# Kernel optimization log

Hardware: AMD Instinct MI355X
Metric: run time of the kernel (lower is better)

The kernel has to match this reference:

```python
import jax, jax.numpy as jnp
import numpy as np

E, H, V, P, RAW = 512, 1024, 12000, 36, 2048
B, L = 128, 21

def setup_inputs() -> dict:
    key = jax.random.key(0)
    ks = jax.random.split(key, 16)
    n = lambda k, sh: (0.02 * jax.random.normal(k, sh)).astype(jnp.float32)
    z = lambda sh: jnp.zeros(sh, jnp.float32)
    return {
        "images_features": jax.random.normal(ks[0], (B, P, RAW), dtype=jnp.float32),
        "encoded_captions": jax.random.randint(ks[1], (B, L), 0, V),
        "caption_lengths": L,
        "W_img": n(ks[2], (RAW, H)), "b_img": z((H,)),
        "W_glob": n(ks[3], (H, E)), "b_glob": z((E,)),
        "W_ih1": n(ks[4], (2 * E + H, 4 * H)), "W_hh1": n(ks[5], (H, 4 * H)),
        "b_ih1": z((4 * H,)), "b_hh1": z((4 * H,)),
        "Wx_gate": n(ks[6], (2 * E + H, H)), "bx_gate": z((H,)),
        "Wh_gate": n(ks[7], (H, H)), "bh_gate": z((H,)),
        "W_ih2": n(ks[8], (2 * H, 4 * H)), "W_hh2": n(ks[9], (H, 4 * H)),
        "b_ih2": z((4 * H,)), "b_hh2": z((4 * H,)),
        "Wv": n(ks[10], (H, P)), "bv": z((P,)),
        "Ws": n(ks[11], (H, P)), "bs": z((P,)),
        "Wg": n(ks[12], (H, P)),
        "wh": n(ks[13], (P,)),
        "emb": n(ks[14], (V, E)),
        "W_fc": n(ks[15], (H, V)), "b_fc": z((V,)),
    }

def _lstm(x, h, c, W_ih, W_hh, b_ih, b_hh):
    # torch LSTMCell gate order: i, f, g, o
    g = x @ W_ih + b_ih + h @ W_hh + b_hh
    i, f, gg, o = jnp.split(g, 4, axis=-1)
    c_new = jax.nn.sigmoid(f) * c + jax.nn.sigmoid(i) * jnp.tanh(gg)
    h_new = jax.nn.sigmoid(o) * jnp.tanh(c_new)
    return h_new, c_new

def reference(images_features, encoded_captions, caption_lengths, W_img, b_img,
              W_glob, b_glob, W_ih1, W_hh1, b_ih1, b_hh1, Wx_gate, bx_gate,
              Wh_gate, bh_gate, W_ih2, W_hh2, b_ih2, b_hh2, Wv, bv, Ws, bs,
              Wg, wh, emb, W_fc, b_fc):
    Bsz = images_features.shape[0]
    Hd = W_hh1.shape[0]
    T = int(caption_lengths) - 1
    Vfeat = jax.nn.relu(images_features @ W_img + b_img)            # (B,P,H)
    glob = jax.nn.relu(jnp.mean(Vfeat, axis=1) @ W_glob + b_glob)   # (B,E)
    img_proj = Vfeat @ Wv + bv                                      # (B,P,P) loop-invariant
    word_embs = emb[encoded_captions[:, :T]]                        # (B,T,E)

    def step(carry, we):
        h1, c1, h2, c2 = carry
        xt = jnp.concatenate([h2, glob, we], axis=-1)               # (B, H+2E)
        h1n, c1n = _lstm(xt, h1, c1, W_ih1, W_hh1, b_ih1, b_hh1)
        sen_gate = jax.nn.sigmoid(xt @ Wx_gate + bx_gate + h1 @ Wh_gate + bh_gate)
        st = sen_gate * jnp.tanh(c1n)                               # visual sentinel
        ht_proj = h1n @ Wg                                          # (B,P)
        z = jnp.tanh(img_proj + ht_proj[:, :, None]) @ wh           # (B,P)
        alpha = jax.nn.softmax(z, axis=1)                           # (B,P)
        context = jnp.einsum('bp,bph->bh', alpha, Vfeat)            # (B,H)
        att_vs = jnp.tanh(st @ Ws + bs + ht_proj) @ wh              # (B,)
        alpha_hat = jax.nn.softmax(jnp.concatenate([z, att_vs[:, None]], axis=1), axis=1)
        beta = alpha_hat[:, -1:]                                    # (B,1)
        c_hat = beta * st + (1.0 - beta) * context
        h2n, c2n = _lstm(jnp.concatenate([c_hat, h1n], axis=-1), h2, c2,
                         W_ih2, W_hh2, b_ih2, b_hh2)
        score = (c_hat + h2n) @ W_fc + b_fc                         # (B,V)
        return (h1n, c1n, h2n, c2n), (score, alpha, beta)

    zeros = jnp.zeros((Bsz, Hd), images_features.dtype)
    init = (zeros, zeros, zeros, zeros)
    _, (preds, alphas, betas) = jax.lax.scan(step, init, jnp.swapaxes(word_embs, 0, 1))
    return (jnp.swapaxes(preds, 0, 1),   # (B,T,V)
            jnp.swapaxes(alphas, 0, 1),  # (B,T,P)
            jnp.swapaxes(betas, 0, 1))   # (B,T,1)
```

## Files before the change

### kernel.cpp

```cpp
#include <hip/hip_runtime.h>
#include <hip/hip_bf16.h>
#include <math.h>

typedef __attribute__((ext_vector_type(4))) float f32x4;
typedef __attribute__((ext_vector_type(8))) short bf16x8;

constexpr int kB = 128, kT = 20, kH = 1024, kE = 512, kP = 36, kRaw = 2048, kV = 12000;

__device__ __forceinline__ float sigf(float x) { return 1.0f / (1.0f + expf(-x)); }

#define AS1C const __attribute__((address_space(1))) void*
#define AS3P __attribute__((address_space(3))) void*

constexpr int NZ1 = 2 * kB * kH / 4;
constexpr int NZ2 = 2 * kB * kH * 2 / 16;
constexpr int NCV = kB * kP * kRaw / 4;
constexpr int NPV = 64 * 1024 * 2 / 16;
constexpr int NPF = 32 * 1024 * 2 / 16;
constexpr int NPB = 5120;
constexpr int NGE = kB * kT * kE;

__global__ __launch_bounds__(256) void prep_small(
    float* c1z, uint4* h1z, const float* images, __hip_bfloat16* imagesb,
    uint4* wtv, uint4* wtfc_pad,
    const float* b_ih1, const float* b_hh1, const float* bx, const float* bh,
    const float* b_ih2, const float* b_hh2, float* bias_g1, float* bias_g2,
    const int* caps, const float* emb, __hip_bfloat16* wembb) {
  long idx = (long)blockIdx.x * 256 + threadIdx.x;
  if (idx < NZ1) { reinterpret_cast<float4*>(c1z)[idx] = make_float4(0, 0, 0, 0); return; }
  idx -= NZ1;
  if (idx < NZ2) { h1z[idx] = make_uint4(0, 0, 0, 0); return; }
  idx -= NZ2;
  if (idx < NCV) {
    float4 v = reinterpret_cast<const float4*>(images)[idx];
    __hip_bfloat16* d = imagesb + idx * 4;
    d[0] = __float2bfloat16(v.x); d[1] = __float2bfloat16(v.y);
    d[2] = __float2bfloat16(v.z); d[3] = __float2bfloat16(v.w);
    return;
  }
  idx -= NCV;
  if (idx < NPV) { wtv[idx] = make_uint4(0, 0, 0, 0); return; }
  idx -= NPV;
  if (idx < NPF) { wtfc_pad[idx] = make_uint4(0, 0, 0, 0); return; }
  idx -= NPF;
  if (idx < NPB) {
    int i = (int)idx;
    if (i < 4096) {
      bias_g1[i] = b_ih1[i] + b_hh1[i];
      bias_g2[i] = b_ih2[i] + b_hh2[i];
    } else {
      bias_g1[i] = bx[i - 4096] + bh[i - 4096];
    }
    return;
  }
  idx -= NPB;
  if (idx < NGE) {
    int e = (int)(idx % kE);
    int bt = (int)(idx / kE);
    int t = bt % kT;
    int b = bt / kT;
    int tok = caps[b * (kT + 1) + t];
    wembb[idx] = __float2bfloat16(emb[(size_t)tok * kE + e]);
  }
}

struct TJob {
  const float* src; __hip_bfloat16* dst;
  int ld_src, K, N, lddst, koff, noff, blk_off, nbx;
};
struct TAll { TJob job[11]; int njobs; int total_blocks; };

__global__ __launch_bounds__(256) void transpose_all(TAll ta) {
  __shared__ float t[32][33];
  int bid = blockIdx.x;
  int ji = 0;
  while (ji + 1 < ta.njobs && bid >= ta.job[ji + 1].blk_off) ++ji;
  const TJob& J = ta.job[ji];
  int lbid = bid - J.blk_off;
  int n0 = (lbid % J.nbx) * 32, k0 = (lbid / J.nbx) * 32;
  int tx = threadIdx.x & 31, ty = threadIdx.x >> 5;
  #pragma unroll
  for (int i = 0; i < 32; i += 8) {
    int k = k0 + ty + i, n = n0 + tx;
    t[ty + i][tx] = (k < J.K && n < J.N) ? J.src[(size_t)k * J.ld_src + n] : 0.0f;
  }
  __syncthreads();
  #pragma unroll
  for (int i = 0; i < 32; i += 8) {
    int n = n0 + ty + i, k = k0 + tx;
    if (n < J.N && k < J.K)
      J.dst[(size_t)(n + J.noff) * J.lddst + k + J.koff] = __float2bfloat16(t[tx][ty + i]);
  }
}

struct SegB { const __hip_bfloat16* A; int lda; int kstart; int kend; };
struct GemmBArgs {
  SegB seg[4]; int nseg;
  const __hip_bfloat16* WT; int ldk;
  const float* bias;
  float* C; __hip_bfloat16* C16; int ldc; int N; int Ktot; int act;
};

__global__ __launch_bounds__(256) void gemm_bf16(GemmBArgs ga) {
  __shared__ char lds[98304];
  const int bm = blockIdx.y * 64;
  const int bn = blockIdx.x * 64;
  const int tid = threadIdx.x;
  const int lane = tid & 63;
  const int w = tid >> 6;
  const int wr = w >> 1, wc = w & 1;

  int rowS[4], scbS[4], dstS[4];
  #pragma unroll
  for (int j = 0; j < 4; ++j) {
    int off = ((j * 4 + w) * 64 + lane) * 16;
    int row = off >> 8, colb = off & 255;
    rowS[j] = row;
    scbS[j] = colb ^ ((row & 7) << 4);
    dstS[j] = (j * 4 + w) * 1024;
  }

  f32x4 acc[2][2] = {};
  const int nit = ga.Ktot >> 7;

  auto stage = [&](int it, int buf) {
    const int k0 = it << 7;
    int si = 0;
    while (k0 >= ga.seg[si].kend) ++si;
    const __hip_bfloat16* Aseg = ga.seg[si].A;
    const int lda = ga.seg[si].lda;
    const int ks = k0 - ga.seg[si].kstart;
    char* baseA = lds + buf * 32768;
    char* baseB = baseA + 16384;
    #pragma unroll
    for (int j = 0; j < 4; ++j) {
      const __hip_bfloat16* sA = Aseg + (size_t)(bm + rowS[j]) * lda + ks + (scbS[j] >> 1);
      __builtin_amdgcn_global_load_lds((AS1C)sA, (AS3P)(baseA + dstS[j]), 16, 0, 0);
      const __hip_bfloat16* sB = ga.WT + (size_t)(bn + rowS[j]) * ga.ldk + k0 + (scbS[j] >> 1);
      __builtin_amdgcn_global_load_lds((AS1C)sB, (AS3P)(baseB + dstS[j]), 16, 0, 0);
    }
  };

  auto compute = [&](int buf) {
    const char* baseA = lds + buf * 32768;
    const char* baseB = baseA + 16384;
    #pragma unroll
    for (int kk = 0; kk < 4; ++kk) {
      bf16x8 a[2], b[2];
      #pragma unroll
      for (int f = 0; f < 2; ++f) {
        int row = wr * 32 + f * 16 + (lane & 15);
        int cb = kk * 64 + (lane >> 4) * 16;
        a[f] = *(const bf16x8*)(baseA + row * 256 + (cb ^ ((row & 7) << 4)));
        int nl = wc * 32 + f * 16 + (lane & 15);
        b[f] = *(const bf16x8*)(baseB + nl * 256 + (cb ^ ((nl & 7) << 4)));
      }
      #pragma unroll
      for (int fm = 0; fm < 2; ++fm)
        #pragma unroll
        for (int fn = 0; fn < 2; ++fn)
          acc[fm][fn] = __builtin_amdgcn_mfma_f32_16x16x32_bf16(a[fm], b[fn], acc[fm][fn], 0, 0, 0);
    }
  };

  stage(0, 0);
  stage(1, 1);
  asm volatile("s_waitcnt vmcnt(8)" ::: "memory");
  __builtin_amdgcn_s_barrier();
  int cbuf = 0;
  for (int it = 0; it < nit; ++it) {
    if (it + 2 < nit) {
      int sb = cbuf + 2; if (sb >= 3) sb -= 3;
      stage(it + 2, sb);
    }
    compute(cbuf);
    if (it + 1 < nit) {
      if (it + 2 < nit) asm volatile("s_waitcnt vmcnt(8)" ::: "memory");
      else              asm volatile("s_waitcnt vmcnt(0)" ::: "memory");
      __builtin_amdgcn_s_barrier();
    }
    ++cbuf; if (cbuf == 3) cbuf = 0;
  }

  #pragma unroll
  for (int fm = 0; fm < 2; ++fm) {
    int rbase = bm + wr * 32 + fm * 16 + (lane >> 4) * 4;
    #pragma unroll
    for (int fn = 0; fn < 2; ++fn) {
      int col = bn + wc * 32 + fn * 16 + (lane & 15);
      if (col >= ga.N) continue;
      float bv = ga.bias ? ga.bias[col] : 0.0f;
      #pragma unroll
      for (int j = 0; j < 4; ++j) {
        float v = acc[fm][fn][j] + bv;
        if (ga.act == 1) v = fmaxf(v, 0.0f);
        size_t off = (size_t)(rbase + j) * ga.ldc + col;
        if (ga.C) ga.C[off] = v;
        if (ga.C16) ga.C16[off] = __float2bfloat16(v);
      }
    }
  }
}

struct G128Args {
  const __hip_bfloat16* A; int lda;
  const __hip_bfloat16* WT; int ldk;
  const float* bias;
  float* C; __hip_bfloat16* C16; int ldc; int N; int Ktot; int act; int cmap;
};

__global__ __launch_bounds__(256) void gemm128(G128Args ga) {
  __shared__ char lds[98304];
  const int gx = gridDim.x;
  const int nwg = gx * gridDim.y;
  int bid = blockIdx.y * gx + blockIdx.x;
  int q = nwg >> 3, r = nwg & 7;
  int xc = bid & 7, yq = bid >> 3;
  int swz = (xc < r ? xc * (q + 1) : r * (q + 1) + (xc - r) * q) + yq;
  const int bn = (swz % gx) * 128;
  const int bm = (swz / gx) * 128;

  const int tid = threadIdx.x;
  const int lane = tid & 63;
  const int w = tid >> 6;
  const int wr = w >> 1, wc = w & 1;

  int rowS[4], scbS[4], dstS[4];
  #pragma unroll
  for (int j = 0; j < 4; ++j) {
    int off = ((j * 4 + w) * 64 + lane) * 16;
    int row = off >> 7, colb = off & 127;
    rowS[j] = row;
    scbS[j] = colb ^ ((row & 7) << 4);
    dstS[j] = (j * 4 + w) * 1024;
  }

  f32x4 acc[4][4] = {};
  const int nit = ga.Ktot >> 6;

  auto stage = [&](int it, int buf) {
    const int k0 = it << 6;
    char* baseA = lds + buf * 32768;
    char* baseB = baseA + 16384;
    #pragma unroll
    for (int j = 0; j < 4; ++j) {
      const __hip_bfloat16* sA = ga.A + (size_t)(bm + rowS[j]) * ga.lda + k0 + (scbS[j] >> 1);
      __builtin_amdgcn_global_load_lds((AS1C)sA, (AS3P)(baseA + dstS[j]), 16, 0, 0);
      const __hip_bfloat16* sB = ga.WT + (size_t)(bn + rowS[j]) * ga.ldk + k0 + (scbS[j] >> 1);
      __builtin_amdgcn_global_load_lds((AS1C)sB, (AS3P)(baseB + dstS[j]), 16, 0, 0);
    }
  };

  auto compute = [&](int buf) {
    const char* baseA = lds + buf * 32768;
    const char* baseB = baseA + 16384;
    #pragma unroll
    for (int kk = 0; kk < 2; ++kk) {
      bf16x8 a[4], b[4];
      int cb = kk * 64 + (lane >> 4) * 16;
      #pragma unroll
      for (int f = 0; f < 4; ++f) {
        int row = wr * 64 + f * 16 + (lane & 15);
        a[f] = *(const bf16x8*)(baseA + row * 128 + (cb ^ ((row & 7) << 4)));
        int nl = wc * 64 + f * 16 + (lane & 15);
        b[f] = *(const bf16x8*)(baseB + nl * 128 + (cb ^ ((nl & 7) << 4)));
      }
      #pragma unroll
      for (int fm = 0; fm < 4; ++fm)
        #pragma unroll
        for (int fn = 0; fn < 4; ++fn)
          acc[fm][fn] = __builtin_amdgcn_mfma_f32_16x16x32_bf16(a[fm], b[fn], acc[fm][fn], 0, 0, 0);
    }
  };

  stage(0, 0);
  stage(1, 1);
  asm volatile("s_waitcnt vmcnt(8)" ::: "memory");
  __builtin_amdgcn_s_barrier();
  int cbuf = 0;
  for (int it = 0; it < nit; ++it) {
    if (it + 2 < nit) {
      int sb = cbuf + 2; if (sb >= 3) sb -= 3;
      stage(it + 2, sb);
    }
    compute(cbuf);
    if (it + 1 < nit) {
      if (it + 2 < nit) asm volatile("s_waitcnt vmcnt(8)" ::: "memory");
      else              asm volatile("s_waitcnt vmcnt(0)" ::: "memory");
      __builtin_amdgcn_s_barrier();
    }
    ++cbuf; if (cbuf == 3) cbuf = 0;
  }

  #pragma unroll
  for (int fm = 0; fm < 4; ++fm) {
    int rbase = bm + wr * 64 + fm * 16 + (lane >> 4) * 4;
    #pragma unroll
    for (int fn = 0; fn < 4; ++fn) {
      int col = bn + wc * 64 + fn * 16 + (lane & 15);
      if (col >= ga.N) continue;
      float bv = ga.bias ? ga.bias[col] : 0.0f;
      #pragma unroll
      for (int j = 0; j < 4; ++j) {
        float v = acc[fm][fn][j] + bv;
        if (ga.act == 1) v = fmaxf(v, 0.0f);
        int m = rbase + j;
        size_t off = ga.cmap == 1
            ? (size_t)(m & 127) * ga.ldc + (size_t)(m >> 7) * kV + col
            : (size_t)m * ga.ldc + col;
        if (ga.C) ga.C[off] = v;
        if (ga.C16) ga.C16[off] = __float2bfloat16(v);
      }
    }
  }
}

__global__ __launch_bounds__(256) void mean_p(const float* __restrict__ Vfeat,
                                              __hip_bfloat16* __restrict__ meanVb) {
  int idx = blockIdx.x * 256 + threadIdx.x;
  if (idx >= kB * kH) return;
  int b = idx >> 10, h = idx & 1023;
  float sm = 0.0f;
  for (int p = 0; p < kP; ++p) sm += Vfeat[((size_t)b * kP + p) * kH + h];
  meanVb[idx] = __float2bfloat16(sm * (1.0f / kP));
}

__global__ __launch_bounds__(256) void step1_fused(
    const float* __restrict__ g, float* __restrict__ c1,
    __hip_bfloat16* __restrict__ h1b,
    const float* __restrict__ img_proj, const float* __restrict__ Vfeat,
    const float* __restrict__ Wg, const float* __restrict__ Ws,
    const float* __restrict__ bs, const float* __restrict__ wh,
    float* __restrict__ c_hat, __hip_bfloat16* __restrict__ c_hatb,
    float* __restrict__ out_alphas, float* __restrict__ out_betas, int t) {
  const int b = blockIdx.x;
  const int tid = threadIdx.x;
  const int lane = tid & 63;
  const int w = tid >> 6;
  __shared__ float sh_h1[kH];
  __shared__ float sh_st[kH];
  __shared__ float wsum[4][36];
  __shared__ float htp[36];
  __shared__ float stp[36];
  __shared__ float alpha[kP];
  __shared__ float sred[4];

  const float* gr = g + (size_t)b * 5120;
  #pragma unroll
  for (int i = 0; i < 4; ++i) {
    int h = tid + i * 256;
    float ig = sigf(gr[h]);
    float fg = sigf(gr[kH + h]);
    float gg = tanhf(gr[2 * kH + h]);
    float og = sigf(gr[3 * kH + h]);
    int idx = b * kH + h;
    float c = fg * c1[idx] + ig * gg;
    float tc = tanhf(c);
    float hn = og * tc;
    c1[idx] = c;
    h1b[idx] = __float2bfloat16(hn);
    sh_h1[h] = hn;
    sh_st[h] = sigf(gr[4 * kH + h]) * tc;
  }
  __syncthreads();

  #pragma unroll
  for (int pass = 0; pass < 2; ++pass) {
    const float* vec = pass == 0 ? sh_h1 : sh_st;
    const float* W = pass == 0 ? Wg : Ws;
    float pg[36];
    #pragma unroll
    for (int j = 0; j < 36; ++j) pg[j] = 0.0f;
    #pragma unroll
    for (int i = 0; i < 4; ++i) {
      int hh = tid + i * 256;
      float hv = vec[hh];
      const float4* wrow = reinterpret_cast<const float4*>(W + (size_t)hh * 36);
      #pragma unroll
      for (int r = 0; r < 9; ++r) {
        float4 wv = wrow[r];
        pg[4 * r + 0] = fmaf(hv, wv.x, pg[4 * r + 0]);
        pg[4 * r + 1] = fmaf(hv, wv.y, pg[4 * r + 1]);
        pg[4 * r + 2] = fmaf(hv, wv.z, pg[4 * r + 2]);
        pg[4 * r + 3] = fmaf(hv, wv.w, pg[4 * r + 3]);
      }
    }
    #pragma unroll
    for (int j = 0; j < 36; ++j) {
      float v = pg[j];
      #pragma unroll
      for (int off = 32; off > 0; off >>= 1) v += __shfl_down(v, off, 64);
      if (lane == 0) wsum[w][j] = v;
    }
    __syncthreads();
    if (tid < 36) {
      float s = wsum[0][tid] + wsum[1][tid] + wsum[2][tid] + wsum[3][tid];
      if (pass == 0) htp[tid] = s; else stp[tid] = s;
    }
    __syncthreads();
  }

  if (w == 0) {
    float zz_r = -3.0e38f;
    if (lane < kP) {
      const float* ip = img_proj + ((size_t)b * kP + lane) * kP;
      float acc = 0.0f;
      #pragma unroll
      for (int j = 0; j < kP; ++j) acc = fmaf(tanhf(ip[j] + htp[j]), wh[j], acc);
      zz_r = acc;
    }
    float m = zz_r;
    #pragma unroll
    for (int off = 32; off > 0; off >>= 1) m = fmaxf(m, __shfl_xor(m, off, 64));
    float e = (lane < kP) ? expf(zz_r - m) : 0.0f;
    float s = e;
    #pragma unroll
    for (int off = 32; off > 0; off >>= 1) s += __shfl_xor(s, off, 64);
    if (lane < kP) alpha[lane] = e / s;
    if (lane == 0) { sred[2] = m; sred[3] = s; }
  } else if (w == 1) {
    float tv = 0.0f;
    if (lane < kP) tv = tanhf(stp[lane] + bs[lane] + htp[lane]) * wh[lane];
    #pragma unroll
    for (int off = 32; off > 0; off >>= 1) tv += __shfl_xor(tv, off, 64);
    if (lane == 0) sred[0] = tv;
  }
  __syncthreads();
  if (tid == 0) {
    float av = sred[0], m = sred[2], s = sred[3];
    float m2 = fmaxf(m, av);
    float eb = expf(av - m2);
    float beta = eb / (s * expf(m - m2) + eb);
    sred[1] = beta;
    out_betas[b * kT + t] = beta;
  }
  __syncthreads();
  if (tid < kP) out_alphas[((size_t)b * kT + t) * kP + tid] = alpha[tid];
  const float beta = sred[1];
  #pragma unroll
  for (int i = 0; i < 4; ++i) {
    int h = tid + i * 256;
    float ctx = 0.0f;
    for (int p = 0; p < kP; ++p) ctx = fmaf(alpha[p], Vfeat[((size_t)b * kP + p) * kH + h], ctx);
    float v = beta * sh_st[h] + (1.0f - beta) * ctx;
    c_hat[(size_t)b * kH + h] = v;
    c_hatb[(size_t)b * kH + h] = __float2bfloat16(v);
  }
}

__global__ __launch_bounds__(256) void lstm2_elem(const float* __restrict__ g,
                                                  float* __restrict__ c2,
                                                  __hip_bfloat16* __restrict__ h2b,
                                                  const float* __restrict__ c_hat,
                                                  __hip_bfloat16* __restrict__ sbufb) {
  int idx = blockIdx.x * 256 + threadIdx.x;
  if (idx >= kB * kH) return;
  int b = idx >> 10, h = idx & 1023;
  const float* gr = g + (size_t)b * 4 * kH;
  float ig = sigf(gr[h]);
  float fg = sigf(gr[kH + h]);
  float gg = tanhf(gr[2 * kH + h]);
  float og = sigf(gr[3 * kH + h]);
  float c = fg * c2[idx] + ig * gg;
  float hn = og * tanhf(c);
  c2[idx] = c;
  h2b[idx] = __float2bfloat16(hn);
  sbufb[idx] = __float2bfloat16(c_hat[idx] + hn);
}

extern "C" void kernel_launch(void* const* d_in, const int* in_sizes, int n_in,
                              void* d_out, int out_size, void* d_ws, size_t ws_size,
                              hipStream_t stream) {
  const float* images  = (const float*)d_in[0];
  const int*   caps    = (const int*)d_in[1];
  const float* W_img   = (const float*)d_in[3];
  const float* b_img   = (const float*)d_in[4];
  const float* W_glob  = (const float*)d_in[5];
  const float* b_glob  = (const float*)d_in[6];
  const float* W_ih1   = (const float*)d_in[7];
  const float* W_hh1   = (const float*)d_in[8];
  const float* b_ih1   = (const float*)d_in[9];
  const float* b_hh1   = (const float*)d_in[10];
  const float* Wx_gate = (const float*)d_in[11];
  const float* bx_gate = (const float*)d_in[12];
  const float* Wh_gate = (const float*)d_in[13];
  const float* bh_gate = (const float*)d_in[14];
  const float* W_ih2   = (const float*)d_in[15];
  const float* W_hh2   = (const float*)d_in[16];
  const float* b_ih2   = (const float*)d_in[17];
  const float* b_hh2   = (const float*)d_in[18];
  const float* Wv      = (const float*)d_in[19];
  const float* bv      = (const float*)d_in[20];
  const float* Ws_     = (const float*)d_in[21];
  const float* bs_     = (const float*)d_in[22];
  const float* Wg      = (const float*)d_in[23];
  const float* wh      = (const float*)d_in[24];
  const float* emb     = (const float*)d_in[25];
  const float* W_fc    = (const float*)d_in[26];
  const float* b_fc    = (const float*)d_in[27];

  float* out = (float*)d_out;
  float* out_alphas = out + (size_t)kB * kT * kV;
  float* out_betas  = out_alphas + (size_t)kB * kT * kP;

  char* base = (char*)d_ws;
  auto alloc = [&](size_t bytes) {
    char* p = base;
    base += (bytes + 255) & ~(size_t)255;
    return p;
  };
  float*          Vfeat   = (float*)alloc((size_t)kB * kP * kH * 4);
  __hip_bfloat16* Vfeatb  = (__hip_bfloat16*)alloc((size_t)kB * kP * kH * 2);
  __hip_bfloat16* imagesb = (__hip_bfloat16*)alloc((size_t)kB * kP * kRaw * 2);
  __hip_bfloat16* WTg1    = (__hip_bfloat16*)alloc((size_t)5120 * 3072 * 2);
  __hip_bfloat16* WTg2    = (__hip_bfloat16*)alloc((size_t)4096 * 3072 * 2);
  __hip_bfloat16* WTfc    = (__hip_bfloat16*)alloc((size_t)12032 * 1024 * 2);
  __hip_bfloat16* WTimg   = (__hip_bfloat16*)alloc((size_t)1024 * 2048 * 2);
  __hip_bfloat16* WTglob  = (__hip_bfloat16*)alloc((size_t)512 * 1024 * 2);
  __hip_bfloat16* WTv     = (__hip_bfloat16*)alloc((size_t)64 * 1024 * 2);
  __hip_bfloat16* wembb   = (__hip_bfloat16*)alloc((size_t)kB * kT * kE * 2);
  float*          img_proj= (float*)alloc((size_t)kB * kP * kP * 4);
  __hip_bfloat16* globb   = (__hip_bfloat16*)alloc((size_t)kB * kE * 2);
  __hip_bfloat16* meanVb  = (__hip_bfloat16*)alloc((size_t)kB * kH * 2);
  float*          c1      = (float*)alloc((size_t)2 * kB * kH * 4);
  float*          c2      = c1 + kB * kH;
  __hip_bfloat16* h1b     = (__hip_bfloat16*)alloc((size_t)2 * kB * kH * 2);
  __hip_bfloat16* h2b     = h1b + kB * kH;
  float*          g1out   = (float*)alloc((size_t)kB * 5120 * 4);
  float*          chat    = (float*)alloc((size_t)kB * kH * 4);
  __hip_bfloat16* chatb   = (__hip_bfloat16*)alloc((size_t)kB * kH * 2);
  __hip_bfloat16* sbufall = (__hip_bfloat16*)alloc((size_t)kT * kB * kH * 2);
  float*          bias_g1 = (float*)alloc(5120 * 4);
  float*          bias_g2 = (float*)alloc(4096 * 4);

  {
    long total = (long)NZ1 + NZ2 + NCV + NPV + NPF + NPB + NGE;
    int blocks = (int)((total + 255) / 256);
    prep_small<<<blocks, 256, 0, stream>>>(
        c1, (uint4*)h1b, images, imagesb, (uint4*)WTv,
        (uint4*)(WTfc + (size_t)12000 * 1024),
        b_ih1, b_hh1, bx_gate, bh_gate, b_ih2, b_hh2, bias_g1, bias_g2,
        caps, emb, wembb);
  }
  {
    TAll ta = {};
    int off = 0, j = 0;
    auto add = [&](const float* src, int ldsrc, int K, int N, __hip_bfloat16* dst,
                   int lddst, int koff, int noff) {
      int nbx = (N + 31) / 32, nby = (K + 31) / 32;
      ta.job[j] = {src, dst, ldsrc, K, N, lddst, koff, noff, off, nbx};
      off += nbx * nby;
      ++j;
    };
    add(W_img,   kH,     kRaw, kH,     WTimg,  kRaw, 0, 0);
    add(W_glob,  kE,     kH,   kE,     WTglob, kH,   0, 0);
    add(Wv,      kP,     kH,   kP,     WTv,    kH,   0, 0);
    add(W_ih1,   4 * kH, 2048, 4 * kH, WTg1,   3072, 0, 0);
    add(W_hh1,   4 * kH, 1024, 4 * kH, WTg1,   3072, 2048, 0);
    add(Wx_gate, kH,     2048, kH,     WTg1,   3072, 0, 4096);
    add(Wh_gate, kH,     1024, kH,     WTg1,   3072, 2048, 4096);
    add(W_ih2,   4 * kH, 2048, 4 * kH, WTg2,   3072, 0, 0);
    add(W_hh2,   4 * kH, 1024, 4 * kH, WTg2,   3072, 2048, 0);
    add(W_fc,    kV,     kH,   kV,     WTfc,   kH,   0, 0);
    ta.njobs = j;
    ta.total_blocks = off;
    transpose_all<<<off, 256, 0, stream>>>(ta);
  }

  {
    G128Args ga = {};
    ga.A = imagesb; ga.lda = kRaw; ga.WT = WTimg; ga.ldk = kRaw; ga.bias = b_img;
    ga.C = Vfeat; ga.C16 = Vfeatb; ga.ldc = kH; ga.N = kH; ga.Ktot = kRaw;
    ga.act = 1; ga.cmap = 0;
    gemm128<<<dim3(kH / 128, kB * kP / 128), 256, 0, stream>>>(ga);
  }
  mean_p<<<(kB * kH + 255) / 256, 256, 0, stream>>>(Vfeat, meanVb);
  {
    GemmBArgs ga = {};
    ga.seg[0] = {meanVb, kH, 0, kH};
    ga.nseg = 1; ga.WT = WTglob; ga.ldk = kH; ga.bias = b_glob;
    ga.C = nullptr; ga.C16 = globb; ga.ldc = kE; ga.N = kE; ga.Ktot = kH; ga.act = 1;
    gemm_bf16<<<dim3(kE / 64, kB / 64), 256, 0, stream>>>(ga);
  }
  {
    GemmBArgs ga = {};
    ga.seg[0] = {Vfeatb, kH, 0, kH};
    ga.nseg = 1; ga.WT = WTv; ga.ldk = kH; ga.bias = bv;
    ga.C = img_proj; ga.C16 = nullptr; ga.ldc = kP; ga.N = kP; ga.Ktot = kH; ga.act = 0;
    gemm_bf16<<<dim3(1, kB * kP / 64), 256, 0, stream>>>(ga);
  }

  for (int t = 0; t < kT; ++t) {
    {
      GemmBArgs ga = {};
      ga.seg[0] = {h2b, kH, 0, kH};
      ga.seg[1] = {globb, kE, kH, kH + kE};
      ga.seg[2] = {wembb + (size_t)t * kE, kT * kE, kH + kE, 2048};
      ga.seg[3] = {h1b, kH, 2048, 3072};
      ga.nseg = 4; ga.WT = WTg1; ga.ldk = 3072; ga.bias = bias_g1;
      ga.C = g1out; ga.C16 = nullptr; ga.ldc = 5120; ga.N = 5120; ga.Ktot = 3072; ga.act = 0;
      gemm_bf16<<<dim3(5120 / 64, kB / 64), 256, 0, stream>>>(ga);
    }
    step1_fused<<<kB, 256, 0, stream>>>(g1out, c1, h1b, img_proj, Vfeat,
                                        Wg, Ws_, bs_, wh, chat, chatb,
                                        out_alphas, out_betas, t);
    {
      GemmBArgs ga = {};
      ga.seg[0] = {chatb, kH, 0, kH};
      ga.seg[1] = {h1b, kH, kH, 2048};
      ga.seg[2] = {h2b, kH, 2048, 3072};
      ga.nseg = 3; ga.WT = WTg2; ga.ldk = 3072; ga.bias = bias_g2;
      ga.C = g1out; ga.C16 = nullptr; ga.ldc = 4096; ga.N = 4096; ga.Ktot = 3072; ga.act = 0;
      gemm_bf16<<<dim3(4096 / 64, kB / 64), 256, 0, stream>>>(ga);
    }
    lstm2_elem<<<(kB * kH + 255) / 256, 256, 0, stream>>>(
        g1out, c2, h2b, chat, sbufall + (size_t)t * kB * kH);
  }

  {
    G128Args ga = {};
    ga.A = sbufall; ga.lda = kH; ga.WT = WTfc; ga.ldk = kH; ga.bias = b_fc;
    ga.C = out; ga.C16 = nullptr; ga.ldc = kT * kV; ga.N = kV; ga.Ktot = kH;
    ga.act = 0; ga.cmap = 1;
    gemm128<<<dim3(12032 / 128, kT * kB / 128), 256, 0, stream>>>(ga);
  }
}
```

Baseline: 1.829 ms.

## Split-K the per-step gate GEMMs and move to double-buffered LDS

The two recurrent gate GEMMs now launch with a grid z of 2. Each half covers half the K range and writes its partial sums to a separate output slab, and the bias add moves into the following elementwise kernels, which sum the two slabs. This is meant to double the workgroup count for these small 128-row GEMMs, which otherwise fill few CUs. Both GEMM kernels also drop from triple to double buffering (64 KB of LDS) with an extra barrier per iteration, which may allow higher occupancy but shortens prefetch depth and adds extra global traffic for the partial slabs.

```diff
diff --git a/kernel.cpp b/kernel.cpp
--- a/kernel.cpp
+++ b/kernel.cpp
@@ -98,11 +98,11 @@
   SegB seg[4]; int nseg;
   const __hip_bfloat16* WT; int ldk;
   const float* bias;
-  float* C; __hip_bfloat16* C16; int ldc; int N; int Ktot; int act;
+  float* C; __hip_bfloat16* C16; int ldc; int N; int Ktot; int act; int zstride;
 };
 
 __global__ __launch_bounds__(256) void gemm_bf16(GemmBArgs ga) {
-  __shared__ char lds[98304];
+  __shared__ char lds[65536];
   const int bm = blockIdx.y * 64;
   const int bn = blockIdx.x * 64;
   const int tid = threadIdx.x;
@@ -121,7 +121,10 @@
   }
 
   f32x4 acc[2][2] = {};
-  const int nit = ga.Ktot >> 7;
+  const int nz = gridDim.z;
+  const int nit = (ga.Ktot >> 7) / nz;
+  const int it0 = blockIdx.z * nit;
+  float* C = ga.C + (size_t)blockIdx.z * ga.zstride;
 
   auto stage = [&](int it, int buf) {
     const int k0 = it << 7;
@@ -163,23 +166,21 @@
     }
   };
 
-  stage(0, 0);
-  stage(1, 1);
+  stage(it0, 0);
+  stage(it0 + 1, 1);
   asm volatile("s_waitcnt vmcnt(8)" ::: "memory");
   __builtin_amdgcn_s_barrier();
-  int cbuf = 0;
-  for (int it = 0; it < nit; ++it) {
-    if (it + 2 < nit) {
-      int sb = cbuf + 2; if (sb >= 3) sb -= 3;
-      stage(it + 2, sb);
-    }
-    compute(cbuf);
-    if (it + 1 < nit) {
-      if (it + 2 < nit) asm volatile("s_waitcnt vmcnt(8)" ::: "memory");
-      else              asm volatile("s_waitcnt vmcnt(0)" ::: "memory");
+  int cur = 0;
+  for (int i = 0; i < nit; ++i) {
+    compute(cur);
+    __builtin_amdgcn_s_barrier();
+    if (i + 2 < nit) stage(it0 + i + 2, cur);
+    if (i + 1 < nit) {
+      if (i + 2 < nit) asm volatile("s_waitcnt vmcnt(8)" ::: "memory");
+      else             asm volatile("s_waitcnt vmcnt(0)" ::: "memory");
       __builtin_amdgcn_s_barrier();
     }
-    ++cbuf; if (cbuf == 3) cbuf = 0;
+    cur ^= 1;
   }
 
   #pragma unroll
@@ -195,7 +196,7 @@
         float v = acc[fm][fn][j] + bv;
         if (ga.act == 1) v = fmaxf(v, 0.0f);
         size_t off = (size_t)(rbase + j) * ga.ldc + col;
-        if (ga.C) ga.C[off] = v;
+        if (ga.C) C[off] = v;
         if (ga.C16) ga.C16[off] = __float2bfloat16(v);
       }
     }
@@ -210,7 +211,7 @@
 };
 
 __global__ __launch_bounds__(256) void gemm128(G128Args ga) {
-  __shared__ char lds[98304];
+  __shared__ char lds[65536];
   const int gx = gridDim.x;
   const int nwg = gx * gridDim.y;
   int bid = blockIdx.y * gx + blockIdx.x;
@@ -277,19 +278,17 @@
   stage(1, 1);
   asm volatile("s_waitcnt vmcnt(8)" ::: "memory");
   __builtin_amdgcn_s_barrier();
-  int cbuf = 0;
-  for (int it = 0; it < nit; ++it) {
-    if (it + 2 < nit) {
-      int sb = cbuf + 2; if (sb >= 3) sb -= 3;
-      stage(it + 2, sb);
-    }
-    compute(cbuf);
-    if (it + 1 < nit) {
-      if (it + 2 < nit) asm volatile("s_waitcnt vmcnt(8)" ::: "memory");
-      else              asm volatile("s_waitcnt vmcnt(0)" ::: "memory");
+  int cur = 0;
+  for (int i = 0; i < nit; ++i) {
+    compute(cur);
+    __builtin_amdgcn_s_barrier();
+    if (i + 2 < nit) stage(i + 2, cur);
+    if (i + 1 < nit) {
+      if (i + 2 < nit) asm volatile("s_waitcnt vmcnt(8)" ::: "memory");
+      else             asm volatile("s_waitcnt vmcnt(0)" ::: "memory");
       __builtin_amdgcn_s_barrier();
     }
-    ++cbuf; if (cbuf == 3) cbuf = 0;
+    cur ^= 1;
   }
 
   #pragma unroll
@@ -325,9 +324,10 @@
   meanVb[idx] = __float2bfloat16(sm * (1.0f / kP));
 }
 
+constexpr int kSlab1 = kB * 5120;
 __global__ __launch_bounds__(256) void step1_fused(
-    const float* __restrict__ g, float* __restrict__ c1,
-    __hip_bfloat16* __restrict__ h1b,
+    const float* __restrict__ g, const float* __restrict__ bias_g1,
+    float* __restrict__ c1, __hip_bfloat16* __restrict__ h1b,
     const float* __restrict__ img_proj, const float* __restrict__ Vfeat,
     const float* __restrict__ Wg, const float* __restrict__ Ws,
     const float* __restrict__ bs, const float* __restrict__ wh,
@@ -345,14 +345,15 @@
   __shared__ float alpha[kP];
   __shared__ float sred[4];
 
-  const float* gr = g + (size_t)b * 5120;
+  const float* gr0 = g + (size_t)b * 5120;
+  const float* gr1 = gr0 + kSlab1;
   #pragma unroll
   for (int i = 0; i < 4; ++i) {
     int h = tid + i * 256;
-    float ig = sigf(gr[h]);
-    float fg = sigf(gr[kH + h]);
-    float gg = tanhf(gr[2 * kH + h]);
-    float og = sigf(gr[3 * kH + h]);
+    float ig = sigf(gr0[h]           + gr1[h]           + bias_g1[h]);
+    float fg = sigf(gr0[kH + h]      + gr1[kH + h]      + bias_g1[kH + h]);
+    float gg = tanhf(gr0[2 * kH + h] + gr1[2 * kH + h]  + bias_g1[2 * kH + h]);
+    float og = sigf(gr0[3 * kH + h]  + gr1[3 * kH + h]  + bias_g1[3 * kH + h]);
     int idx = b * kH + h;
     float c = fg * c1[idx] + ig * gg;
     float tc = tanhf(c);
@@ -360,7 +361,7 @@
     c1[idx] = c;
     h1b[idx] = __float2bfloat16(hn);
     sh_h1[h] = hn;
-    sh_st[h] = sigf(gr[4 * kH + h]) * tc;
+    sh_st[h] = sigf(gr0[4 * kH + h] + gr1[4 * kH + h] + bias_g1[4 * kH + h]) * tc;
   }
   __syncthreads();
 
@@ -448,7 +449,9 @@
   }
 }
 
+constexpr int kSlab2 = kB * 4096;
 __global__ __launch_bounds__(256) void lstm2_elem(const float* __restrict__ g,
+                                                  const float* __restrict__ bias_g2,
                                                   float* __restrict__ c2,
                                                   __hip_bfloat16* __restrict__ h2b,
                                                   const float* __restrict__ c_hat,
@@ -456,11 +459,12 @@
   int idx = blockIdx.x * 256 + threadIdx.x;
   if (idx >= kB * kH) return;
   int b = idx >> 10, h = idx & 1023;
-  const float* gr = g + (size_t)b * 4 * kH;
-  float ig = sigf(gr[h]);
-  float fg = sigf(gr[kH + h]);
-  float gg = tanhf(gr[2 * kH + h]);
-  float og = sigf(gr[3 * kH + h]);
+  const float* gr0 = g + (size_t)b * 4 * kH;
+  const float* gr1 = gr0 + kSlab2;
+  float ig = sigf(gr0[h]           + gr1[h]           + bias_g2[h]);
+  float fg = sigf(gr0[kH + h]      + gr1[kH + h]      + bias_g2[kH + h]);
+  float gg = tanhf(gr0[2 * kH + h] + gr1[2 * kH + h]  + bias_g2[2 * kH + h]);
+  float og = sigf(gr0[3 * kH + h]  + gr1[3 * kH + h]  + bias_g2[3 * kH + h]);
   float c = fg * c2[idx] + ig * gg;
   float hn = og * tanhf(c);
   c2[idx] = c;
@@ -526,7 +530,7 @@
   float*          c2      = c1 + kB * kH;
   __hip_bfloat16* h1b     = (__hip_bfloat16*)alloc((size_t)2 * kB * kH * 2);
   __hip_bfloat16* h2b     = h1b + kB * kH;
-  float*          g1out   = (float*)alloc((size_t)kB * 5120 * 4);
+  float*          g1out   = (float*)alloc((size_t)2 * kB * 5120 * 4);
   float*          chat    = (float*)alloc((size_t)kB * kH * 4);
   __hip_bfloat16* chatb   = (__hip_bfloat16*)alloc((size_t)kB * kH * 2);
   __hip_bfloat16* sbufall = (__hip_bfloat16*)alloc((size_t)kT * kB * kH * 2);
@@ -580,14 +584,14 @@
     ga.seg[0] = {meanVb, kH, 0, kH};
     ga.nseg = 1; ga.WT = WTglob; ga.ldk = kH; ga.bias = b_glob;
     ga.C = nullptr; ga.C16 = globb; ga.ldc = kE; ga.N = kE; ga.Ktot = kH; ga.act = 1;
-    gemm_bf16<<<dim3(kE / 64, kB / 64), 256, 0, stream>>>(ga);
+    gemm_bf16<<<dim3(kE / 64, kB / 64, 1), 256, 0, stream>>>(ga);
   }
   {
     GemmBArgs ga = {};
     ga.seg[0] = {Vfeatb, kH, 0, kH};
     ga.nseg = 1; ga.WT = WTv; ga.ldk = kH; ga.bias = bv;
     ga.C = img_proj; ga.C16 = nullptr; ga.ldc = kP; ga.N = kP; ga.Ktot = kH; ga.act = 0;
-    gemm_bf16<<<dim3(1, kB * kP / 64), 256, 0, stream>>>(ga);
+    gemm_bf16<<<dim3(1, kB * kP / 64, 1), 256, 0, stream>>>(ga);
   }
 
   for (int t = 0; t < kT; ++t) {
@@ -597,11 +601,12 @@
       ga.seg[1] = {globb, kE, kH, kH + kE};
       ga.seg[2] = {wembb + (size_t)t * kE, kT * kE, kH + kE, 2048};
       ga.seg[3] = {h1b, kH, 2048, 3072};
-      ga.nseg = 4; ga.WT = WTg1; ga.ldk = 3072; ga.bias = bias_g1;
-      ga.C = g1out; ga.C16 = nullptr; ga.ldc = 5120; ga.N = 5120; ga.Ktot = 3072; ga.act = 0;
-      gemm_bf16<<<dim3(5120 / 64, kB / 64), 256, 0, stream>>>(ga);
-    }
-    step1_fused<<<kB, 256, 0, stream>>>(g1out, c1, h1b, img_proj, Vfeat,
+      ga.nseg = 4; ga.WT = WTg1; ga.ldk = 3072; ga.bias = nullptr;
+      ga.C = g1out; ga.C16 = nullptr; ga.ldc = 5120; ga.N = 5120; ga.Ktot = 3072;
+      ga.act = 0; ga.zstride = kSlab1;
+      gemm_bf16<<<dim3(5120 / 64, kB / 64, 2), 256, 0, stream>>>(ga);
+    }
+    step1_fused<<<kB, 256, 0, stream>>>(g1out, bias_g1, c1, h1b, img_proj, Vfeat,
                                         Wg, Ws_, bs_, wh, chat, chatb,
                                         out_alphas, out_betas, t);
     {
@@ -609,12 +614,13 @@
       ga.seg[0] = {chatb, kH, 0, kH};
       ga.seg[1] = {h1b, kH, kH, 2048};
       ga.seg[2] = {h2b, kH, 2048, 3072};
-      ga.nseg = 3; ga.WT = WTg2; ga.ldk = 3072; ga.bias = bias_g2;
-      ga.C = g1out; ga.C16 = nullptr; ga.ldc = 4096; ga.N = 4096; ga.Ktot = 3072; ga.act = 0;
-      gemm_bf16<<<dim3(4096 / 64, kB / 64), 256, 0, stream>>>(ga);
+      ga.nseg = 3; ga.WT = WTg2; ga.ldk = 3072; ga.bias = nullptr;
+      ga.C = g1out; ga.C16 = nullptr; ga.ldc = 4096; ga.N = 4096; ga.Ktot = 3072;
+      ga.act = 0; ga.zstride = kSlab2;
+      gemm_bf16<<<dim3(4096 / 64, kB / 64, 2), 256, 0, stream>>>(ga);
     }
     lstm2_elem<<<(kB * kH + 255) / 256, 256, 0, stream>>>(
-        g1out, c2, h2b, chat, sbufall + (size_t)t * kB * kH);
+        g1out, bias_g2, c2, h2b, chat, sbufall + (size_t)t * kB * kH);
   }
 
   {
```

Measured after the change: 1.588 ms. 1.15x faster.
